# Performance work log

Hardware: AMD Instinct MI355X
Metric: run time of the kernel (lower is better)

The kernel has to match this reference:

```python
import jax, jax.numpy as jnp
import numpy as np

N_PROTS = 2048
MOLS_PER_PROT = 8
N_MOLS = N_PROTS * MOLS_PER_PROT
DIM = 768
MARGIN = 0.5


def setup_inputs() -> dict:
    key = jax.random.key(0)
    k1, k2, k3 = jax.random.split(key, 3)
    prot_emb = jax.random.normal(k1, (N_PROTS, DIM), dtype=jnp.float32)
    mol_emb = jax.random.normal(k2, (N_MOLS, DIM), dtype=jnp.float32)
    # L2-normalize like typical CLIP-style retrieval embeddings
    prot_emb = prot_emb / jnp.linalg.norm(prot_emb, axis=1, keepdims=True)
    mol_emb = mol_emb / jnp.linalg.norm(mol_emb, axis=1, keepdims=True)
    # block-structured labels: protein i paired with mols [8i, 8i+8)
    rows = jnp.repeat(jnp.arange(N_PROTS), MOLS_PER_PROT)
    cols = jnp.arange(N_MOLS)
    labels = jnp.zeros((N_PROTS, N_MOLS), dtype=jnp.float32).at[rows, cols].set(1.0)
    # pIC50 values in [2, 10]
    pic50_matrix = 2.0 + 8.0 * jax.random.uniform(k3, (N_PROTS, N_MOLS), dtype=jnp.float32)
    logit_scale = jnp.float32(1.0 / 0.07)
    return {"prot_emb": prot_emb, "mol_emb": mol_emb, "labels": labels,
            "pic50_matrix": pic50_matrix, "logit_scale": logit_scale}


def reference(prot_emb, mol_emb, labels, pic50_matrix, logit_scale):
    n_prots = prot_emb.shape[0]
    n_mols = mol_emb.shape[0]
    sim = jnp.matmul(prot_emb, mol_emb.T) * logit_scale  # [n_prots, n_mols]

    # affinity-weighted InfoNCE (prot -> mol)
    pic50_norm = jnp.clip((pic50_matrix - 2.0) / 8.0, 0.0, 1.0)
    pos_w = labels * pic50_norm
    pos_w = pos_w / (pos_w.sum(axis=1, keepdims=True) + 1e-8)
    loss_p2m = -jnp.sum(pos_w * jax.nn.log_softmax(sim, axis=1)) / n_prots

    # mol -> prot NLL
    mol_labels = jnp.argmax(labels, axis=0)  # [n_mols]
    lsm_m2p = jax.nn.log_softmax(sim.T, axis=1)  # [n_mols, n_prots]
    loss_m2p = -jnp.mean(lsm_m2p[jnp.arange(n_mols), mol_labels])

    # pairwise margin-ranking among positives (exactly MOLS_PER_PROT positives per protein)
    P = MOLS_PER_PROT
    _, pos_idx = jax.lax.top_k(labels, P)  # [n_prots, P] indices of positives
    pos_pic = jnp.take_along_axis(pic50_matrix, pos_idx, axis=1)  # [n_prots, P]
    pos_sc = jnp.take_along_axis(sim, pos_idx, axis=1)            # [n_prots, P]
    dp = pos_pic[:, :, None] - pos_pic[:, None, :]  # [n_prots, P, P]
    ds = pos_sc[:, :, None] - pos_sc[:, None, :]
    pair = jnp.where(dp > 0, jax.nn.relu(MARGIN - ds),
                     jnp.where(dp < 0, jax.nn.relu(MARGIN + ds), 0.0))
    upper = jnp.triu(jnp.ones((P, P), dtype=bool), k=1)  # unordered pairs j<k
    n_pairs = n_prots * (P * (P - 1) // 2)
    ranking_loss = jnp.sum(jnp.where(upper[None], pair, 0.0)) / n_pairs

    # negative push-down
    neg_loss = jnp.mean(jax.nn.relu(sim * (1.0 - labels)))

    total = loss_p2m + loss_m2p + 0.5 * ranking_loss + 0.1 * neg_loss
    return (total, loss_p2m, loss_m2p, ranking_loss, neg_loss)
```

## Files before the change

### kernel.cpp

```cpp
#include <hip/hip_runtime.h>
#include <hip/hip_bf16.h>
#include <math.h>

#define N_PROTS 2048
#define N_MOLS  16384
#define DIM     768
#define SHIFT   16.0f
#define MARGIN  0.5f

typedef __attribute__((ext_vector_type(8))) short short8;
typedef __attribute__((ext_vector_type(4))) float f32x4;
typedef __attribute__((ext_vector_type(4))) unsigned short us4;
typedef __attribute__((ext_vector_type(8))) unsigned short us8;

__device__ __forceinline__ unsigned short bf16rnd(float x) {
    unsigned int u = __float_as_uint(x);
    u += 0x7fffu + ((u >> 16) & 1u);
    return (unsigned short)(u >> 16);
}

__device__ __forceinline__ void gload16(const void* g, void* l) {
    __builtin_amdgcn_global_load_lds(
        (const __attribute__((address_space(1))) unsigned int*)g,
        (__attribute__((address_space(3))) unsigned int*)l, 16, 0, 0);
}

__device__ __forceinline__ int sig4(int x) { return (x + (x >> 2)) & 3; }

#define ACC_FLOATS 34824
#define PROT_BF_OFF_B 139296ull
#define PROT_BF_BYTES (2048ull*768*2)
#define MOL_BF_OFF_B  (PROT_BF_OFF_B + PROT_BF_BYTES)
#define MOL_BF_BYTES  (16384ull*768*2)
#define WS_NEED       (MOL_BF_OFF_B + MOL_BF_BYTES)

__global__ __launch_bounds__(256)
void convert_bf16(const float* __restrict__ prot, const float* __restrict__ mol,
                  unsigned short* __restrict__ protBf, unsigned short* __restrict__ molBf,
                  float* __restrict__ wsZero)
{
    const size_t PROT_G = (size_t)N_PROTS * DIM / 8;
    size_t t = (size_t)blockIdx.x * 256 + threadIdx.x;
    if (t < (ACC_FLOATS + 3) / 4) {
        float4 z = {0.f, 0.f, 0.f, 0.f};
        ((float4*)wsZero)[t] = z;
    }
    const float* src;
    unsigned short* dst;
    if (t < PROT_G) { src = prot + t * 8; dst = protBf + t * 8; }
    else            { size_t u = t - PROT_G; src = mol + u * 8; dst = molBf + u * 8; }
    float4 v0 = ((const float4*)src)[0];
    float4 v1 = ((const float4*)src)[1];
    us8 o;
    o[0] = bf16rnd(v0.x); o[1] = bf16rnd(v0.y); o[2] = bf16rnd(v0.z); o[3] = bf16rnd(v0.w);
    o[4] = bf16rnd(v1.x); o[5] = bf16rnd(v1.y); o[6] = bf16rnd(v1.z); o[7] = bf16rnd(v1.w);
    *(us8*)dst = o;
}

__global__ __launch_bounds__(512)
void sim_pass_bf16_v5b(const unsigned short* __restrict__ protBf,
                       const unsigned short* __restrict__ molBf,
                       const float* __restrict__ scale_p,
                       float* __restrict__ row_se, float* __restrict__ col_se,
                       float* __restrict__ pos_sim, float* __restrict__ scalars)
{
    __shared__ unsigned short As[3][256][32];
    __shared__ unsigned short Bs[3][256][32];
    __shared__ float redBuf[8];

    const int tid = threadIdx.x;
    const int bid  = blockIdx.x;
    const int xcd  = bid & 7;
    const int sl8  = bid >> 3;
    const int bx   = xcd * 8 + (sl8 & 7);
    const int by   = sl8 >> 3;
    const int rowBase = by * 256;
    const int colBase = bx * 256;

    const int wave = tid >> 6;
    const int lane = tid & 63;
    const int wm = wave >> 2;
    const int wn = wave & 3;
    const int l15 = lane & 15;
    const int q   = lane >> 4;

    const int rsub = lane >> 2;
    const int cs   = lane & 3;
    const int csrc = (cs ^ sig4(rsub)) << 3;
    const unsigned short* aP =
        protBf + (size_t)(rowBase + wave * 32 + rsub) * DIM + csrc;
    const unsigned short* bP =
        molBf  + (size_t)(colBase + wave * 32 + rsub) * DIM + csrc;

#define STAGE_A(sl, kt) do { \
    gload16(aP + (size_t)(kt) * 32,                    &As[sl][wave * 32][0]);      \
    gload16(aP + (size_t)(kt) * 32 + (size_t)16 * DIM, &As[sl][wave * 32 + 16][0]); \
} while (0)
#define STAGE_B(sl, kt) do { \
    gload16(bP + (size_t)(kt) * 32,                    &Bs[sl][wave * 32][0]);      \
    gload16(bP + (size_t)(kt) * 32 + (size_t)16 * DIM, &Bs[sl][wave * 32 + 16][0]); \
} while (0)

    f32x4 acc[8][4];
#pragma unroll
    for (int i = 0; i < 8; ++i)
#pragma unroll
        for (int j = 0; j < 4; ++j) acc[i][j] = (f32x4){0.f, 0.f, 0.f, 0.f};

    STAGE_A(0, 0); STAGE_B(0, 0);
    STAGE_A(1, 1); STAGE_B(1, 1);

    const int fArow = wm * 128 + l15;
    const int fBrow = wn * 64 + l15;
    const int fsw   = (q ^ sig4(l15)) << 3;

#pragma unroll 1
    for (int kt = 0; kt < 24; ++kt) {
        const int db  = kt % 3;
        const int s2  = (kt + 2) % 3;
        const int kt2 = (kt + 2 < 24) ? (kt + 2) : (kt - 10);

        asm volatile("s_waitcnt vmcnt(4)" ::: "memory");
        __builtin_amdgcn_s_barrier();
        __builtin_amdgcn_sched_barrier(0);

        short8 aF[4], bF[4];
#pragma unroll
        for (int ni = 0; ni < 4; ++ni)
            bF[ni] = *(const short8*)&Bs[db][fBrow + ni * 16][fsw];
#pragma unroll
        for (int mi = 0; mi < 4; ++mi)
            aF[mi] = *(const short8*)&As[db][fArow + mi * 16][fsw];
        STAGE_A(s2, kt2);
        asm volatile("s_waitcnt lgkmcnt(0)" ::: "memory");
        __builtin_amdgcn_sched_barrier(0);
        __builtin_amdgcn_s_setprio(1);
#pragma unroll
        for (int mi = 0; mi < 4; ++mi)
#pragma unroll
            for (int ni = 0; ni < 4; ++ni)
                acc[mi][ni] = __builtin_amdgcn_mfma_f32_16x16x32_bf16(
                    aF[mi], bF[ni], acc[mi][ni], 0, 0, 0);
        __builtin_amdgcn_s_setprio(0);

#pragma unroll
        for (int mi = 0; mi < 4; ++mi)
            aF[mi] = *(const short8*)&As[db][fArow + 64 + mi * 16][fsw];
        STAGE_B(s2, kt2);
        asm volatile("s_waitcnt lgkmcnt(0)" ::: "memory");
        __builtin_amdgcn_sched_barrier(0);
        __builtin_amdgcn_s_setprio(1);
#pragma unroll
        for (int mi = 0; mi < 4; ++mi)
#pragma unroll
            for (int ni = 0; ni < 4; ++ni)
                acc[4 + mi][ni] = __builtin_amdgcn_mfma_f32_16x16x32_bf16(
                    aF[mi], bF[ni], acc[4 + mi][ni], 0, 0, 0);
        __builtin_amdgcn_s_setprio(0);
    }
    asm volatile("s_waitcnt vmcnt(0)" ::: "memory");
#undef STAGE_A
#undef STAGE_B

    const float scale = scale_p[0];
    float csum[4] = {0.f, 0.f, 0.f, 0.f};
    float rl = 0.f;
#pragma unroll
    for (int mi = 0; mi < 8; ++mi) {
        float rs[4] = {0.f, 0.f, 0.f, 0.f};
#pragma unroll
        for (int ni = 0; ni < 4; ++ni) {
#pragma unroll
            for (int r = 0; r < 4; ++r) {
                float sim = acc[mi][ni][r] * scale;
                float e = __expf(sim - SHIFT);
                rs[r] += e;
                csum[ni] += e;
                rl += fmaxf(sim, 0.f);
                int rg = rowBase + wm * 128 + mi * 16 + q * 4 + r;
                int cg = colBase + wn * 64 + ni * 16 + l15;
                if ((cg >> 3) == rg) pos_sim[cg] = sim;
            }
        }
#pragma unroll
        for (int r = 0; r < 4; ++r) {
            float v = rs[r];
            v += __shfl_xor(v, 1); v += __shfl_xor(v, 2);
            v += __shfl_xor(v, 4); v += __shfl_xor(v, 8);
            if (l15 == 0)
                atomicAdd(&row_se[rowBase + wm * 128 + mi * 16 + q * 4 + r], v);
        }
    }
#pragma unroll
    for (int ni = 0; ni < 4; ++ni) {
        float v = csum[ni];
        v += __shfl_xor(v, 16); v += __shfl_xor(v, 32);
        if (q == 0)
            atomicAdd(&col_se[colBase + wn * 64 + ni * 16 + l15], v);
    }
#pragma unroll
    for (int m = 1; m < 64; m <<= 1) rl += __shfl_xor(rl, m);
    if (lane == 0) redBuf[wave] = rl;
    __syncthreads();
    if (tid == 0) {
        float sv = 0.f;
#pragma unroll
        for (int w = 0; w < 8; ++w) sv += redBuf[w];
        atomicAdd(&scalars[0], sv);
    }
}

__global__ __launch_bounds__(256, 2)
void sim_pass(const float* __restrict__ prot, const float* __restrict__ mol,
              const float* __restrict__ scale_p,
              float* __restrict__ row_se, float* __restrict__ col_se,
              float* __restrict__ pos_sim, float* __restrict__ scalars)
{
    __shared__ unsigned short As[128][32];
    __shared__ unsigned short Bs[128][32];
    __shared__ float redBuf[4];

    const int tid = threadIdx.x;
    const int rowBase = blockIdx.y * 128;
    const int colBase = blockIdx.x * 128;
    const int wave = tid >> 6;
    const int lane = tid & 63;
    const int wr = (wave >> 1) * 64;
    const int wc = (wave & 1) * 64;
    const int l15 = lane & 15;
    const int q   = lane >> 4;

    f32x4 acc[4][4];
#pragma unroll
    for (int i = 0; i < 4; ++i)
#pragma unroll
        for (int j = 0; j < 4; ++j) acc[i][j] = (f32x4){0.f, 0.f, 0.f, 0.f};

    const float* aBase = prot + (size_t)rowBase * DIM;
    const float* bBase = mol  + (size_t)colBase * DIM;
    float4 aReg[4], bReg[4];
#pragma unroll
    for (int i = 0; i < 4; ++i) {
        int f = tid + 256 * i;
        int row = f >> 3, c4 = f & 7;
        aReg[i] = *(const float4*)(aBase + (size_t)row * DIM + (c4 << 2));
        bReg[i] = *(const float4*)(bBase + (size_t)row * DIM + (c4 << 2));
    }
#pragma unroll 1
    for (int s = 0; s < DIM / 32; ++s) {
#pragma unroll
        for (int i = 0; i < 4; ++i) {
            int f = tid + 256 * i;
            int row = f >> 3, c4 = f & 7;
            us4 av, bv;
            av.x = bf16rnd(aReg[i].x); av.y = bf16rnd(aReg[i].y);
            av.z = bf16rnd(aReg[i].z); av.w = bf16rnd(aReg[i].w);
            bv.x = bf16rnd(bReg[i].x); bv.y = bf16rnd(bReg[i].y);
            bv.z = bf16rnd(bReg[i].z); bv.w = bf16rnd(bReg[i].w);
            *(us4*)&As[row][c4 << 2] = av;
            *(us4*)&Bs[row][c4 << 2] = bv;
        }
        __syncthreads();
        if (s + 1 < DIM / 32) {
            int k0 = (s + 1) * 32;
#pragma unroll
            for (int i = 0; i < 4; ++i) {
                int f = tid + 256 * i;
                int row = f >> 3, c4 = f & 7;
                aReg[i] = *(const float4*)(aBase + (size_t)row * DIM + k0 + (c4 << 2));
                bReg[i] = *(const float4*)(bBase + (size_t)row * DIM + k0 + (c4 << 2));
            }
        }
        short8 aF[4], bF[4];
#pragma unroll
        for (int mi = 0; mi < 4; ++mi) aF[mi] = *(const short8*)&As[wr + mi * 16 + l15][q * 8];
#pragma unroll
        for (int ni = 0; ni < 4; ++ni) bF[ni] = *(const short8*)&Bs[wc + ni * 16 + l15][q * 8];
#pragma unroll
        for (int mi = 0; mi < 4; ++mi)
#pragma unroll
            for (int ni = 0; ni < 4; ++ni)
                acc[mi][ni] = __builtin_amdgcn_mfma_f32_16x16x32_bf16(aF[mi], bF[ni], acc[mi][ni], 0, 0, 0);
        __syncthreads();
    }

    const float scale = scale_p[0];
    float rsum[4][4];
    float csum[4] = {0.f, 0.f, 0.f, 0.f};
    float rl = 0.f;
#pragma unroll
    for (int mi = 0; mi < 4; ++mi)
#pragma unroll
        for (int r = 0; r < 4; ++r) rsum[mi][r] = 0.f;
#pragma unroll
    for (int mi = 0; mi < 4; ++mi) {
#pragma unroll
        for (int ni = 0; ni < 4; ++ni) {
#pragma unroll
            for (int r = 0; r < 4; ++r) {
                float sim = acc[mi][ni][r] * scale;
                float e = __expf(sim - SHIFT);
                rsum[mi][r] += e;
                csum[ni] += e;
                rl += fmaxf(sim, 0.f);
                int rg = rowBase + wr + mi * 16 + q * 4 + r;
                int cg = colBase + wc + ni * 16 + l15;
                if ((cg >> 3) == rg) pos_sim[cg] = sim;
            }
        }
    }
#pragma unroll
    for (int mi = 0; mi < 4; ++mi) {
#pragma unroll
        for (int r = 0; r < 4; ++r) {
            float v = rsum[mi][r];
            v += __shfl_xor(v, 1); v += __shfl_xor(v, 2);
            v += __shfl_xor(v, 4); v += __shfl_xor(v, 8);
            if (l15 == 0)
                atomicAdd(&row_se[rowBase + wr + mi * 16 + q * 4 + r], v);
        }
    }
#pragma unroll
    for (int ni = 0; ni < 4; ++ni) {
        float v = csum[ni];
        v += __shfl_xor(v, 16); v += __shfl_xor(v, 32);
        if (q == 0)
            atomicAdd(&col_se[colBase + wc + ni * 16 + l15], v);
    }
#pragma unroll
    for (int m = 1; m < 64; m <<= 1) rl += __shfl_xor(rl, m);
    if (lane == 0) redBuf[wave] = rl;
    __syncthreads();
    if (tid == 0)
        atomicAdd(&scalars[0], redBuf[0] + redBuf[1] + redBuf[2] + redBuf[3]);
}

__global__ __launch_bounds__(256)
void finalize_mb(const float* __restrict__ row_se, const float* __restrict__ col_se,
                 const float* __restrict__ pos_sim, const float* __restrict__ pic50,
                 float* __restrict__ scalars, float* __restrict__ out)
{
    int j = blockIdx.x * 256 + threadIdx.x;
    float m2p = SHIFT + __logf(col_se[j]) - pos_sim[j];

    float p2m = 0.f, rank = 0.f, prelu = 0.f;
    if ((j & 7) == 0) {
        int i = j >> 3;
        float s[8], pc[8], pr[8];
#pragma unroll
        for (int p = 0; p < 8; ++p) {
            s[p]  = pos_sim[j + p];
            pr[p] = pic50[(size_t)i * N_MOLS + j + p];
            float x = (pr[p] - 2.0f) * 0.125f;
            pc[p] = fminf(fmaxf(x, 0.f), 1.f);
            prelu += fmaxf(s[p], 0.f);
        }
        float wsum = 1e-8f;
#pragma unroll
        for (int p = 0; p < 8; ++p) wsum += pc[p];
        float lse = SHIFT + __logf(row_se[i]);
        float accp = 0.f;
#pragma unroll
        for (int p = 0; p < 8; ++p) accp += pc[p] * (lse - s[p]);
        p2m = accp / wsum;
#pragma unroll
        for (int a = 0; a < 8; ++a)
#pragma unroll
            for (int b = a + 1; b < 8; ++b) {
                float dp = pr[a] - pr[b];
                float ds = s[a] - s[b];
                float v = (dp > 0.f) ? fmaxf(MARGIN - ds, 0.f)
                        : ((dp < 0.f) ? fmaxf(MARGIN + ds, 0.f) : 0.f);
                rank += v;
            }
    }
#pragma unroll
    for (int m = 1; m < 64; m <<= 1) {
        m2p   += __shfl_xor(m2p, m);
        p2m   += __shfl_xor(p2m, m);
        rank  += __shfl_xor(rank, m);
        prelu += __shfl_xor(prelu, m);
    }
    __shared__ float rbuf[4][4];
    const int wave = threadIdx.x >> 6, lane = threadIdx.x & 63;
    if (lane == 0) { rbuf[wave][0] = m2p; rbuf[wave][1] = p2m;
                     rbuf[wave][2] = rank; rbuf[wave][3] = prelu; }
    __syncthreads();
    if (threadIdx.x == 0) {
        float a = 0, b = 0, c = 0, d = 0;
        for (int w = 0; w < 4; ++w) { a += rbuf[w][0]; b += rbuf[w][1];
                                      c += rbuf[w][2]; d += rbuf[w][3]; }
        atomicAdd(&scalars[2], a);
        atomicAdd(&scalars[1], b);
        atomicAdd(&scalars[3], c);
        atomicAdd(&scalars[4], d);
        __threadfence();
        float old = atomicAdd(&scalars[7], 1.0f);
        if (old == (float)(N_MOLS / 256 - 1)) {
            float s0 = atomicAdd(&scalars[0], 0.0f);
            float s1 = atomicAdd(&scalars[1], 0.0f);
            float s2 = atomicAdd(&scalars[2], 0.0f);
            float s3 = atomicAdd(&scalars[3], 0.0f);
            float s4 = atomicAdd(&scalars[4], 0.0f);
            float relu_neg = s0 - s4;
            float p2mv  = s1 / (float)N_PROTS;
            float m2pv  = s2 / (float)N_MOLS;
            float rankv = s3 / ((float)N_PROTS * 28.0f);
            float negv  = relu_neg / ((float)N_PROTS * (float)N_MOLS);
            out[0] = p2mv + m2pv + 0.5f * rankv + 0.1f * negv;
            out[1] = p2mv;
            out[2] = m2pv;
            out[3] = rankv;
            out[4] = negv;
        }
    }
}

extern "C" void kernel_launch(void* const* d_in, const int* in_sizes, int n_in,
                              void* d_out, int out_size, void* d_ws, size_t ws_size,
                              hipStream_t stream) {
    const float* prot   = (const float*)d_in[0];
    const float* mol    = (const float*)d_in[1];
    const float* pic50  = (const float*)d_in[3];
    const float* lscale = (const float*)d_in[4];

    float* ws      = (float*)d_ws;
    float* row_se  = ws;
    float* col_se  = ws + 2048;
    float* pos_sim = ws + 2048 + 16384;
    float* scalars = ws + 34816;

    if (ws_size >= WS_NEED) {
        unsigned short* protBf = (unsigned short*)((char*)d_ws + PROT_BF_OFF_B);
        unsigned short* molBf  = (unsigned short*)((char*)d_ws + MOL_BF_OFF_B);
        size_t groups = ((size_t)N_PROTS + N_MOLS) * DIM / 8;
        convert_bf16<<<(unsigned)(groups / 256), 256, 0, stream>>>(prot, mol, protBf, molBf, ws);
        sim_pass_bf16_v5b<<<512, 512, 0, stream>>>(protBf, molBf, lscale, row_se, col_se, pos_sim, scalars);
    } else {
        hipMemsetAsync(d_ws, 0, (size_t)ACC_FLOATS * sizeof(float), stream);
        dim3 grid(N_MOLS / 128, N_PROTS / 128);
        sim_pass<<<grid, 256, 0, stream>>>(prot, mol, lscale, row_se, col_se, pos_sim, scalars);
    }
    finalize_mb<<<N_MOLS / 256, 256, 0, stream>>>(row_se, col_se, pos_sim, pic50, scalars, (float*)d_out);
}
```

Baseline: 381.7 us.

## Switch similarity GEMM from bf16 to fp8 scaled MFMA with double buffering

Embeddings are now converted to fp8 instead of bf16, and the similarity matmul uses the 16x16x128 f8f6f4 scaled MFMA with unit scales. The K loop becomes 6 steps of 128 with a simpler two-buffer LDS pipeline and XOR swizzle, replacing the 24-step triple-buffered bf16 loop. This halves operand bytes and raises MFMA throughput per instruction. The cost is lower precision in the logits, where errors are amplified by the logit scale of about 14 before exp and log-softmax. It also gives up the finer vmcnt-based overlap of the old pipeline.

```diff
diff --git a/kernel.cpp b/kernel.cpp
--- a/kernel.cpp
+++ b/kernel.cpp
@@ -11,7 +11,8 @@
 typedef __attribute__((ext_vector_type(8))) short short8;
 typedef __attribute__((ext_vector_type(4))) float f32x4;
 typedef __attribute__((ext_vector_type(4))) unsigned short us4;
-typedef __attribute__((ext_vector_type(8))) unsigned short us8;
+typedef __attribute__((ext_vector_type(4))) int i32x4;
+typedef __attribute__((ext_vector_type(8))) int i32x8;
 
 __device__ __forceinline__ unsigned short bf16rnd(float x) {
     unsigned int u = __float_as_uint(x);
@@ -25,19 +26,17 @@
         (__attribute__((address_space(3))) unsigned int*)l, 16, 0, 0);
 }
 
-__device__ __forceinline__ int sig4(int x) { return (x + (x >> 2)) & 3; }
-
 #define ACC_FLOATS 34824
-#define PROT_BF_OFF_B 139296ull
-#define PROT_BF_BYTES (2048ull*768*2)
-#define MOL_BF_OFF_B  (PROT_BF_OFF_B + PROT_BF_BYTES)
-#define MOL_BF_BYTES  (16384ull*768*2)
-#define WS_NEED       (MOL_BF_OFF_B + MOL_BF_BYTES)
+#define PROT_F8_OFF_B 139296ull
+#define PROT_F8_BYTES (2048ull*768)
+#define MOL_F8_OFF_B  (PROT_F8_OFF_B + PROT_F8_BYTES)
+#define MOL_F8_BYTES  (16384ull*768)
+#define WS_NEED       (MOL_F8_OFF_B + MOL_F8_BYTES)
 
 __global__ __launch_bounds__(256)
-void convert_bf16(const float* __restrict__ prot, const float* __restrict__ mol,
-                  unsigned short* __restrict__ protBf, unsigned short* __restrict__ molBf,
-                  float* __restrict__ wsZero)
+void convert_fp8(const float* __restrict__ prot, const float* __restrict__ mol,
+                 unsigned char* __restrict__ protF8, unsigned char* __restrict__ molF8,
+                 float* __restrict__ wsZero)
 {
     const size_t PROT_G = (size_t)N_PROTS * DIM / 8;
     size_t t = (size_t)blockIdx.x * 256 + threadIdx.x;
@@ -46,26 +45,28 @@
         ((float4*)wsZero)[t] = z;
     }
     const float* src;
-    unsigned short* dst;
-    if (t < PROT_G) { src = prot + t * 8; dst = protBf + t * 8; }
-    else            { size_t u = t - PROT_G; src = mol + u * 8; dst = molBf + u * 8; }
+    unsigned char* dst;
+    if (t < PROT_G) { src = prot + t * 8; dst = protF8 + t * 8; }
+    else            { size_t u = t - PROT_G; src = mol + u * 8; dst = molF8 + u * 8; }
     float4 v0 = ((const float4*)src)[0];
     float4 v1 = ((const float4*)src)[1];
-    us8 o;
-    o[0] = bf16rnd(v0.x); o[1] = bf16rnd(v0.y); o[2] = bf16rnd(v0.z); o[3] = bf16rnd(v0.w);
-    o[4] = bf16rnd(v1.x); o[5] = bf16rnd(v1.y); o[6] = bf16rnd(v1.z); o[7] = bf16rnd(v1.w);
-    *(us8*)dst = o;
+    int w0 = __builtin_amdgcn_cvt_pk_fp8_f32(v0.x, v0.y, 0,  false);
+    w0     = __builtin_amdgcn_cvt_pk_fp8_f32(v0.z, v0.w, w0, true);
+    int w1 = __builtin_amdgcn_cvt_pk_fp8_f32(v1.x, v1.y, 0,  false);
+    w1     = __builtin_amdgcn_cvt_pk_fp8_f32(v1.z, v1.w, w1, true);
+    int2 o; o.x = w0; o.y = w1;
+    *(int2*)dst = o;
 }
 
 __global__ __launch_bounds__(512)
-void sim_pass_bf16_v5b(const unsigned short* __restrict__ protBf,
-                       const unsigned short* __restrict__ molBf,
-                       const float* __restrict__ scale_p,
-                       float* __restrict__ row_se, float* __restrict__ col_se,
-                       float* __restrict__ pos_sim, float* __restrict__ scalars)
+void sim_pass_fp8(const unsigned char* __restrict__ protF8,
+                  const unsigned char* __restrict__ molF8,
+                  const float* __restrict__ scale_p,
+                  float* __restrict__ row_se, float* __restrict__ col_se,
+                  float* __restrict__ pos_sim, float* __restrict__ scalars)
 {
-    __shared__ unsigned short As[3][256][32];
-    __shared__ unsigned short Bs[3][256][32];
+    __shared__ unsigned char As[2][256][128];
+    __shared__ unsigned char Bs[2][256][128];
     __shared__ float redBuf[8];
 
     const int tid = threadIdx.x;
@@ -84,22 +85,23 @@
     const int l15 = lane & 15;
     const int q   = lane >> 4;
 
-    const int rsub = lane >> 2;
-    const int cs   = lane & 3;
-    const int csrc = (cs ^ sig4(rsub)) << 3;
-    const unsigned short* aP =
-        protBf + (size_t)(rowBase + wave * 32 + rsub) * DIM + csrc;
-    const unsigned short* bP =
-        molBf  + (size_t)(colBase + wave * 32 + rsub) * DIM + csrc;
-
-#define STAGE_A(sl, kt) do { \
-    gload16(aP + (size_t)(kt) * 32,                    &As[sl][wave * 32][0]);      \
-    gload16(aP + (size_t)(kt) * 32 + (size_t)16 * DIM, &As[sl][wave * 32 + 16][0]); \
+    const int r8    = lane >> 3;
+    const int c8    = lane & 7;
+    const int srcsw = ((c8 ^ r8) << 4);
+    const unsigned char* aP =
+        protF8 + (size_t)(rowBase + wave * 32 + r8) * DIM + srcsw;
+    const unsigned char* bP =
+        molF8  + (size_t)(colBase + wave * 32 + r8) * DIM + srcsw;
+
+#define STAGE(buf, kt) do {                                                   \
+    _Pragma("unroll")                                                         \
+    for (int i2 = 0; i2 < 4; ++i2) {                                          \
+        gload16(aP + (size_t)(kt) * 128 + (size_t)i2 * 8 * DIM,               \
+                &As[buf][wave * 32 + i2 * 8][0]);                             \
+        gload16(bP + (size_t)(kt) * 128 + (size_t)i2 * 8 * DIM,               \
+                &Bs[buf][wave * 32 + i2 * 8][0]);                             \
+    }                                                                         \
 } while (0)
-#define STAGE_B(sl, kt) do { \
-    gload16(bP + (size_t)(kt) * 32,                    &Bs[sl][wave * 32][0]);      \
-    gload16(bP + (size_t)(kt) * 32 + (size_t)16 * DIM, &Bs[sl][wave * 32 + 16][0]); \
-} while (0)
 
     f32x4 acc[8][4];
 #pragma unroll
@@ -107,60 +109,43 @@
 #pragma unroll
         for (int j = 0; j < 4; ++j) acc[i][j] = (f32x4){0.f, 0.f, 0.f, 0.f};
 
-    STAGE_A(0, 0); STAGE_B(0, 0);
-    STAGE_A(1, 1); STAGE_B(1, 1);
+    STAGE(0, 0);
 
     const int fArow = wm * 128 + l15;
     const int fBrow = wn * 64 + l15;
-    const int fsw   = (q ^ sig4(l15)) << 3;
+    const int s0 = ((2 * q)     ^ (l15 & 7)) << 4;
+    const int s1 = ((2 * q + 1) ^ (l15 & 7)) << 4;
 
 #pragma unroll 1
-    for (int kt = 0; kt < 24; ++kt) {
-        const int db  = kt % 3;
-        const int s2  = (kt + 2) % 3;
-        const int kt2 = (kt + 2 < 24) ? (kt + 2) : (kt - 10);
-
-        asm volatile("s_waitcnt vmcnt(4)" ::: "memory");
-        __builtin_amdgcn_s_barrier();
-        __builtin_amdgcn_sched_barrier(0);
-
-        short8 aF[4], bF[4];
-#pragma unroll
-        for (int ni = 0; ni < 4; ++ni)
-            bF[ni] = *(const short8*)&Bs[db][fBrow + ni * 16][fsw];
-#pragma unroll
-        for (int mi = 0; mi < 4; ++mi)
-            aF[mi] = *(const short8*)&As[db][fArow + mi * 16][fsw];
-        STAGE_A(s2, kt2);
-        asm volatile("s_waitcnt lgkmcnt(0)" ::: "memory");
-        __builtin_amdgcn_sched_barrier(0);
+    for (int kt = 0; kt < 6; ++kt) {
+        const int cur = kt & 1, nxt = cur ^ 1;
+        __syncthreads();
+        if (kt + 1 < 6) STAGE(nxt, kt + 1);
+
+        i32x8 bF[4];
+#pragma unroll
+        for (int ni = 0; ni < 4; ++ni) {
+            const unsigned char* rp = &Bs[cur][fBrow + ni * 16][0];
+            i32x4 lo = *(const i32x4*)(rp + s0);
+            i32x4 hi = *(const i32x4*)(rp + s1);
+            bF[ni] = (i32x8){lo[0], lo[1], lo[2], lo[3], hi[0], hi[1], hi[2], hi[3]};
+        }
         __builtin_amdgcn_s_setprio(1);
 #pragma unroll
-        for (int mi = 0; mi < 4; ++mi)
+        for (int mi = 0; mi < 8; ++mi) {
+            const unsigned char* rp = &As[cur][fArow + mi * 16][0];
+            i32x4 lo = *(const i32x4*)(rp + s0);
+            i32x4 hi = *(const i32x4*)(rp + s1);
+            i32x8 aF = (i32x8){lo[0], lo[1], lo[2], lo[3], hi[0], hi[1], hi[2], hi[3]};
 #pragma unroll
             for (int ni = 0; ni < 4; ++ni)
-                acc[mi][ni] = __builtin_amdgcn_mfma_f32_16x16x32_bf16(
-                    aF[mi], bF[ni], acc[mi][ni], 0, 0, 0);
+                acc[mi][ni] = __builtin_amdgcn_mfma_scale_f32_16x16x128_f8f6f4(
+                    aF, bF[ni], acc[mi][ni], 0, 0,
+                    0, 0x7F7F7F7F, 0, 0x7F7F7F7F);
+        }
         __builtin_amdgcn_s_setprio(0);
-
-#pragma unroll
-        for (int mi = 0; mi < 4; ++mi)
-            aF[mi] = *(const short8*)&As[db][fArow + 64 + mi * 16][fsw];
-        STAGE_B(s2, kt2);
-        asm volatile("s_waitcnt lgkmcnt(0)" ::: "memory");
-        __builtin_amdgcn_sched_barrier(0);
-        __builtin_amdgcn_s_setprio(1);
-#pragma unroll
-        for (int mi = 0; mi < 4; ++mi)
-#pragma unroll
-            for (int ni = 0; ni < 4; ++ni)
-                acc[4 + mi][ni] = __builtin_amdgcn_mfma_f32_16x16x32_bf16(
-                    aF[mi], bF[ni], acc[4 + mi][ni], 0, 0, 0);
-        __builtin_amdgcn_s_setprio(0);
-    }
-    asm volatile("s_waitcnt vmcnt(0)" ::: "memory");
-#undef STAGE_A
-#undef STAGE_B
+    }
+#undef STAGE
 
     const float scale = scale_p[0];
     float csum[4] = {0.f, 0.f, 0.f, 0.f};
@@ -431,11 +416,11 @@
     float* scalars = ws + 34816;
 
     if (ws_size >= WS_NEED) {
-        unsigned short* protBf = (unsigned short*)((char*)d_ws + PROT_BF_OFF_B);
-        unsigned short* molBf  = (unsigned short*)((char*)d_ws + MOL_BF_OFF_B);
+        unsigned char* protF8 = (unsigned char*)((char*)d_ws + PROT_F8_OFF_B);
+        unsigned char* molF8  = (unsigned char*)((char*)d_ws + MOL_F8_OFF_B);
         size_t groups = ((size_t)N_PROTS + N_MOLS) * DIM / 8;
-        convert_bf16<<<(unsigned)(groups / 256), 256, 0, stream>>>(prot, mol, protBf, molBf, ws);
-        sim_pass_bf16_v5b<<<512, 512, 0, stream>>>(protBf, molBf, lscale, row_se, col_se, pos_sim, scalars);
+        convert_fp8<<<(unsigned)(groups / 256), 256, 0, stream>>>(prot, mol, protF8, molF8, ws);
+        sim_pass_fp8<<<512, 512, 0, stream>>>(protF8, molF8, lscale, row_se, col_se, pos_sim, scalars);
     } else {
         hipMemsetAsync(d_ws, 0, (size_t)ACC_FLOATS * sizeof(float), stream);
         dim3 grid(N_MOLS / 128, N_PROTS / 128);
```

After: 357.0 us. -6.5%, faster.
